# Optimization experiments

Measured on AMD Instinct MI355X. Metric: run time of the kernel, lower is better.

The kernel has to match this reference:

```python
import jax, jax.numpy as jnp
import numpy as np

C = 128
EPS = 1e-5


def _ln(x, g, b):
    m = jnp.mean(x, axis=-1, keepdims=True)
    v = jnp.mean((x - m) ** 2, axis=-1, keepdims=True)
    return (x - m) * jax.lax.rsqrt(v + EPS) * g + b


def setup_inputs() -> dict:
    key = jax.random.key(0)
    ks = jax.random.split(key, 10)
    B, N = 1, 384
    s = 1.0 / np.sqrt(C)
    inp = {
        "z": jax.random.normal(ks[0], (B, N, N, C), dtype=jnp.float32),
        "ln1_g": jnp.ones((C,), jnp.float32),
        "ln1_b": jnp.zeros((C,), jnp.float32),
        "ln2_g": jnp.ones((C,), jnp.float32),
        "ln2_b": jnp.zeros((C,), jnp.float32),
        "Wa": jax.random.uniform(ks[1], (C, C), jnp.float32, -s, s),
        "ba": jnp.zeros((C,), jnp.float32),
        "Wga": jax.random.uniform(ks[2], (C, C), jnp.float32, -s, s),
        "bga": jnp.zeros((C,), jnp.float32),
        "Wb": jax.random.uniform(ks[3], (C, C), jnp.float32, -s, s),
        "bb": jnp.zeros((C,), jnp.float32),
        "Wgb": jax.random.uniform(ks[4], (C, C), jnp.float32, -s, s),
        "bgb": jnp.zeros((C,), jnp.float32),
        "Wg": jax.random.uniform(ks[5], (C, C), jnp.float32, -s, s),
        "bg": jnp.zeros((C,), jnp.float32),
        "Wo": jax.random.uniform(ks[6], (C, C), jnp.float32, -s, s),
        "bo": jnp.zeros((C,), jnp.float32),
    }
    return inp


def reference(z, ln1_g, ln1_b, ln2_g, ln2_b, Wa, ba, Wga, bga, Wb, bb, Wgb, bgb, Wg, bg, Wo, bo):
    # z: (B, i, j, c)
    zn = _ln(z, ln1_g, ln1_b)
    a = (zn @ Wa + ba) * jax.nn.sigmoid(zn @ Wga + bga)      # (B,i,k,c)
    b = (zn @ Wb + bb) * jax.nn.sigmoid(zn @ Wgb + bgb)      # (B,j,k,c)
    gate = jax.nn.sigmoid(zn @ Wg + bg)                      # (B,i,j,c)
    o = jnp.einsum('bikc,bjkc->bijc', a, b)                  # outgoing triangle update
    return gate * (_ln(o, ln2_g, ln2_b) @ Wo + bo)
```

## Files before the change

kernel.cpp:

```cpp
#include <hip/hip_runtime.h>
#include <stdint.h>

typedef _Float16 f16x8 __attribute__((ext_vector_type(8)));
typedef float floatx4 __attribute__((ext_vector_type(4)));

#define RR 147456
#define NC 128
#define NN 384

__device__ inline floatx4 zero4() { floatx4 v; v[0]=0.f; v[1]=0.f; v[2]=0.f; v[3]=0.f; return v; }
__device__ inline float sigmoidf_(float x) { return 1.f / (1.f + __expf(-x)); }

__global__ __launch_bounds__(256) void k0_wt(
    const float* __restrict__ w0, const float* __restrict__ w1,
    const float* __restrict__ w2, const float* __restrict__ w3,
    const float* __restrict__ w4, const float* __restrict__ w5,
    _Float16* __restrict__ wf)
{
  const float* w;
  switch (blockIdx.x) {
    case 0: w = w0; break; case 1: w = w1; break; case 2: w = w2; break;
    case 3: w = w3; break; case 4: w = w4; break; default: w = w5; break;
  }
  _Float16* out = wf + blockIdx.x * 16384;
  const int t = threadIdx.x;
  for (int it = 0; it < 64; ++it) {
    int f = it * 256 + t;
    int j  = f & 7;
    int ln = (f >> 3) & 63;
    int nt = (f >> 9) & 7;
    int k0 = f >> 12;
    int k = k0 * 32 + (ln >> 4) * 8 + j;
    int n = nt * 16 + (ln & 15);
    out[f] = (_Float16)w[k * 128 + n];
  }
}

__global__ __launch_bounds__(256, 4) void k2_ln_gemm(
    const float* __restrict__ z, const float* __restrict__ ln1g, const float* __restrict__ ln1b,
    const _Float16* __restrict__ wf,
    const float* __restrict__ ba, const float* __restrict__ bga,
    const float* __restrict__ bb, const float* __restrict__ bgb,
    const float* __restrict__ bg,
    _Float16* __restrict__ at, _Float16* __restrict__ bt, _Float16* __restrict__ gate)
{
  __shared__ __align__(16) _Float16 zns[64][136];
  const int t = threadIdx.x;
  const int w = t >> 6, lane = t & 63;
  const int l15 = lane & 15, quad = lane >> 4;
  const int r0 = blockIdx.x * 64;
  const int nt0 = w * 2;

  {
    const int g = lane >> 4, h = lane & 15;
    float4 ga = *(const float4*)(ln1g + h*8);
    float4 gb = *(const float4*)(ln1g + h*8 + 4);
    float4 bba = *(const float4*)(ln1b + h*8);
    float4 bbb = *(const float4*)(ln1b + h*8 + 4);
    #pragma unroll
    for (int rr = 0; rr < 4; ++rr) {
      int row = w * 16 + rr * 4 + g;
      const float* zp = z + (size_t)(r0 + row) * NC + h * 8;
      float4 xa = *(const float4*)zp;
      float4 xb = *(const float4*)(zp + 4);
      float s = xa.x + xa.y + xa.z + xa.w + xb.x + xb.y + xb.z + xb.w;
      float q = xa.x*xa.x + xa.y*xa.y + xa.z*xa.z + xa.w*xa.w
              + xb.x*xb.x + xb.y*xb.y + xb.z*xb.z + xb.w*xb.w;
      #pragma unroll
      for (int m = 1; m < 16; m <<= 1) { s += __shfl_xor(s, m); q += __shfl_xor(q, m); }
      float mean = s * (1.f/128.f);
      float var  = q * (1.f/128.f) - mean*mean;
      float rs = rsqrtf(var + 1e-5f);
      union { uint4 u; _Float16 hh[8]; } pk;
      pk.hh[0] = (_Float16)((xa.x - mean) * rs * ga.x + bba.x);
      pk.hh[1] = (_Float16)((xa.y - mean) * rs * ga.y + bba.y);
      pk.hh[2] = (_Float16)((xa.z - mean) * rs * ga.z + bba.z);
      pk.hh[3] = (_Float16)((xa.w - mean) * rs * ga.w + bba.w);
      pk.hh[4] = (_Float16)((xb.x - mean) * rs * gb.x + bbb.x);
      pk.hh[5] = (_Float16)((xb.y - mean) * rs * gb.y + bbb.y);
      pk.hh[6] = (_Float16)((xb.z - mean) * rs * gb.z + bbb.z);
      pk.hh[7] = (_Float16)((xb.w - mean) * rs * gb.w + bbb.w);
      *(uint4*)&zns[row][h * 8] = pk.u;
    }
  }
  __syncthreads();

  const _Float16* pw = wf + lane * 8;
  f16x8 bw[4][2];
  floatx4 acc[4][2];
  union PkU { unsigned int u; _Float16 h[2]; };
  PkU sig[4][2][2];

  auto loadw = [&](int slot) {
    const _Float16* p = pw + slot * 16384;
    #pragma unroll
    for (int k0 = 0; k0 < 4; ++k0)
      #pragma unroll
      for (int j = 0; j < 2; ++j)
        bw[k0][j] = *(const f16x8*)(p + (k0*8 + nt0 + j) * 512);
  };
  auto dogemm = [&]() {
    #pragma unroll
    for (int mt = 0; mt < 4; ++mt) {
      acc[mt][0] = zero4(); acc[mt][1] = zero4();
      #pragma unroll
      for (int k0 = 0; k0 < 4; ++k0) {
        f16x8 af = *(const f16x8*)&zns[mt*16 + l15][k0*32 + quad*8];
        acc[mt][0] = __builtin_amdgcn_mfma_f32_16x16x32_f16(af, bw[k0][0], acc[mt][0], 0, 0, 0);
        acc[mt][1] = __builtin_amdgcn_mfma_f32_16x16x32_f16(af, bw[k0][1], acc[mt][1], 0, 0, 0);
      }
    }
  };
  auto sigpack = [&](const float* big) {
    #pragma unroll
    for (int j = 0; j < 2; ++j) {
      float bgv = big[(nt0 + j)*16 + l15];
      #pragma unroll
      for (int mt = 0; mt < 4; ++mt) {
        sig[mt][j][0].h[0] = (_Float16)sigmoidf_(acc[mt][j][0] + bgv);
        sig[mt][j][0].h[1] = (_Float16)sigmoidf_(acc[mt][j][1] + bgv);
        sig[mt][j][1].h[0] = (_Float16)sigmoidf_(acc[mt][j][2] + bgv);
        sig[mt][j][1].h[1] = (_Float16)sigmoidf_(acc[mt][j][3] + bgv);
      }
    }
  };
  auto combine_store = [&](const float* bia, _Float16* dst) {
    #pragma unroll
    for (int j = 0; j < 2; ++j) {
      int c = (nt0 + j)*16 + l15;
      float bav = bia[c];
      #pragma unroll
      for (int mt = 0; mt < 4; ++mt) {
        union { uint2 u2; _Float16 h[4]; } pk;
        pk.h[0] = (_Float16)((acc[mt][j][0] + bav) * (float)sig[mt][j][0].h[0]);
        pk.h[1] = (_Float16)((acc[mt][j][1] + bav) * (float)sig[mt][j][0].h[1]);
        pk.h[2] = (_Float16)((acc[mt][j][2] + bav) * (float)sig[mt][j][1].h[0]);
        pk.h[3] = (_Float16)((acc[mt][j][3] + bav) * (float)sig[mt][j][1].h[1]);
        *(uint2*)(dst + (size_t)c * RR + r0 + mt*16 + quad*4) = pk.u2;
      }
    }
  };

  loadw(1); dogemm(); sigpack(bga);
  loadw(0); dogemm();
  loadw(3);
  combine_store(ba, at);
  dogemm(); sigpack(bgb);
  loadw(2); dogemm();
  loadw(4);
  combine_store(bb, bt);
  dogemm();
  #pragma unroll
  for (int j = 0; j < 2; ++j) {
    int c = (nt0 + j)*16 + l15;
    float bgv = bg[c];
    #pragma unroll
    for (int mt = 0; mt < 4; ++mt) {
      union { uint2 u2; _Float16 h[4]; } pk;
      #pragma unroll
      for (int r = 0; r < 4; ++r)
        pk.h[r] = (_Float16)sigmoidf_(acc[mt][j][r] + bgv);
      *(uint2*)(gate + (size_t)c * RR + r0 + mt*16 + quad*4) = pk.u2;
    }
  }
}

__global__ __launch_bounds__(256) void k3_tri(
    const _Float16* __restrict__ at, const _Float16* __restrict__ bt, _Float16* __restrict__ o)
{
  __shared__ __align__(16) _Float16 As[128][72];
  __shared__ __align__(16) _Float16 Bs[128][72];
  const int t = threadIdx.x;
  const int w = t >> 6, lane = t & 63, l15 = lane & 15, quad = lane >> 4;
  const int c = blockIdx.y;
  const int i0 = (blockIdx.x / 3) * 128, j0 = (blockIdx.x % 3) * 128;
  const int wi = w >> 1, wj = w & 1;
  const size_t base = (size_t)c * RR;
  const _Float16* A  = at + base;
  const _Float16* Bp = bt + base;

  floatx4 acc[4][4];
  #pragma unroll
  for (int mt = 0; mt < 4; ++mt)
    #pragma unroll
    for (int nt = 0; nt < 4; ++nt) acc[mt][nt] = zero4();

  for (int kk = 0; kk < NN; kk += 64) {
    #pragma unroll
    for (int s2 = 0; s2 < 4; ++s2) {
      int f = s2 * 2048 + t * 8;
      int row = f >> 6, k = f & 63;
      *(uint4*)&As[row][k] = *(const uint4*)(A  + (size_t)(i0 + row) * NN + kk + k);
      *(uint4*)&Bs[row][k] = *(const uint4*)(Bp + (size_t)(j0 + row) * NN + kk + k);
    }
    __syncthreads();
    #pragma unroll
    for (int k0 = 0; k0 < 64; k0 += 32) {
      f16x8 af[4], bfr[4];
      #pragma unroll
      for (int mt = 0; mt < 4; ++mt) af[mt]  = *(const f16x8*)&As[wi*64 + mt*16 + l15][k0 + quad*8];
      #pragma unroll
      for (int nt = 0; nt < 4; ++nt) bfr[nt] = *(const f16x8*)&Bs[wj*64 + nt*16 + l15][k0 + quad*8];
      #pragma unroll
      for (int mt = 0; mt < 4; ++mt)
        #pragma unroll
        for (int nt = 0; nt < 4; ++nt)
          acc[mt][nt] = __builtin_amdgcn_mfma_f32_16x16x32_f16(af[mt], bfr[nt], acc[mt][nt], 0, 0, 0);
    }
    __syncthreads();
  }
  #pragma unroll
  for (int mt = 0; mt < 4; ++mt) {
    #pragma unroll
    for (int r = 0; r < 4; ++r) {
      int i = i0 + wi*64 + mt*16 + quad*4 + r;
      _Float16* orow = o + base + (size_t)i * NN + j0 + wj*64;
      #pragma unroll
      for (int nt = 0; nt < 4; ++nt) orow[nt*16 + l15] = (_Float16)acc[mt][nt][r];
    }
  }
}

__global__ __launch_bounds__(256, 4) void k4_out(
    const _Float16* __restrict__ o, const _Float16* __restrict__ gate,
    const float* __restrict__ ln2g, const float* __restrict__ ln2b,
    const _Float16* __restrict__ wo5, const float* __restrict__ bo,
    float* __restrict__ out)
{
  __shared__ __align__(16) _Float16 osb[64][136];
  const int t = threadIdx.x;
  const int w = t >> 6, lane = t & 63, l15 = lane & 15, quad = lane >> 4;
  const int r0 = blockIdx.x * 64;
  const int nt0 = w * 2;

  #pragma unroll
  for (int it = 0; it < 4; ++it) {
    int f = (it * 256 + t) * 8;
    int cx = f >> 6, p = f & 63;
    f16x8 v = *(const f16x8*)(o + (size_t)cx * RR + r0 + p);
    #pragma unroll
    for (int i = 0; i < 8; ++i) osb[p + i][cx] = v[i];
  }
  __syncthreads();

  {
    const int g = lane >> 4, h = lane & 15;
    float4 ga = *(const float4*)(ln2g + h*8);
    float4 gb = *(const float4*)(ln2g + h*8 + 4);
    float4 bba = *(const float4*)(ln2b + h*8);
    float4 bbb = *(const float4*)(ln2b + h*8 + 4);
    #pragma unroll
    for (int rr = 0; rr < 4; ++rr) {
      int row = w * 16 + rr * 4 + g;
      f16x8 xv = *(const f16x8*)&osb[row][h*8];
      float x0 = (float)xv[0], x1 = (float)xv[1], x2 = (float)xv[2], x3 = (float)xv[3];
      float x4 = (float)xv[4], x5 = (float)xv[5], x6 = (float)xv[6], x7 = (float)xv[7];
      float s = x0+x1+x2+x3+x4+x5+x6+x7;
      float q = x0*x0+x1*x1+x2*x2+x3*x3+x4*x4+x5*x5+x6*x6+x7*x7;
      #pragma unroll
      for (int m = 1; m < 16; m <<= 1) { s += __shfl_xor(s, m); q += __shfl_xor(q, m); }
      float mean = s * (1.f/128.f);
      float var  = q * (1.f/128.f) - mean*mean;
      float rs = rsqrtf(var + 1e-5f);
      union { uint4 u; _Float16 hh[8]; } pk;
      pk.hh[0] = (_Float16)((x0 - mean) * rs * ga.x + bba.x);
      pk.hh[1] = (_Float16)((x1 - mean) * rs * ga.y + bba.y);
      pk.hh[2] = (_Float16)((x2 - mean) * rs * ga.z + bba.z);
      pk.hh[3] = (_Float16)((x3 - mean) * rs * ga.w + bba.w);
      pk.hh[4] = (_Float16)((x4 - mean) * rs * gb.x + bbb.x);
      pk.hh[5] = (_Float16)((x5 - mean) * rs * gb.y + bbb.y);
      pk.hh[6] = (_Float16)((x6 - mean) * rs * gb.z + bbb.z);
      pk.hh[7] = (_Float16)((x7 - mean) * rs * gb.w + bbb.w);
      *(uint4*)&osb[row][h * 8] = pk.u;
    }
  }
  __syncthreads();

  f16x8 bw[4][2];
  {
    const _Float16* p = wo5 + lane * 8;
    #pragma unroll
    for (int k0 = 0; k0 < 4; ++k0)
      #pragma unroll
      for (int j = 0; j < 2; ++j)
        bw[k0][j] = *(const f16x8*)(p + (k0*8 + nt0 + j) * 512);
  }
  floatx4 acc[4][2];
  #pragma unroll
  for (int mt = 0; mt < 4; ++mt) {
    acc[mt][0] = zero4(); acc[mt][1] = zero4();
    #pragma unroll
    for (int k0 = 0; k0 < 4; ++k0) {
      f16x8 af = *(const f16x8*)&osb[mt*16 + l15][k0*32 + quad*8];
      acc[mt][0] = __builtin_amdgcn_mfma_f32_16x16x32_f16(af, bw[k0][0], acc[mt][0], 0, 0, 0);
      acc[mt][1] = __builtin_amdgcn_mfma_f32_16x16x32_f16(af, bw[k0][1], acc[mt][1], 0, 0, 0);
    }
  }

  #pragma unroll
  for (int j = 0; j < 2; ++j) {
    int c = (nt0 + j)*16 + l15;
    float bov = bo[c];
    #pragma unroll
    for (int mt = 0; mt < 4; ++mt) {
      union { uint2 u2; _Float16 h[4]; } gk;
      gk.u2 = *(const uint2*)(gate + (size_t)c * RR + r0 + mt*16 + quad*4);
      #pragma unroll
      for (int r = 0; r < 4; ++r) {
        int rl = mt*16 + quad*4 + r;
        out[(size_t)(r0 + rl) * NC + c] = (float)gk.h[r] * (acc[mt][j][r] + bov);
      }
    }
  }
}

extern "C" void kernel_launch(void* const* d_in, const int* in_sizes, int n_in,
                              void* d_out, int out_size, void* d_ws, size_t ws_size,
                              hipStream_t stream) {
  const float* z    = (const float*)d_in[0];
  const float* l1g  = (const float*)d_in[1];
  const float* l1b  = (const float*)d_in[2];
  const float* l2g  = (const float*)d_in[3];
  const float* l2b  = (const float*)d_in[4];
  const float* Wa   = (const float*)d_in[5];
  const float* ba   = (const float*)d_in[6];
  const float* Wga  = (const float*)d_in[7];
  const float* bga  = (const float*)d_in[8];
  const float* Wb   = (const float*)d_in[9];
  const float* bb   = (const float*)d_in[10];
  const float* Wgb  = (const float*)d_in[11];
  const float* bgb  = (const float*)d_in[12];
  const float* Wg   = (const float*)d_in[13];
  const float* bg   = (const float*)d_in[14];
  const float* Wo   = (const float*)d_in[15];
  const float* bo   = (const float*)d_in[16];

  char* ws = (char*)d_ws;
  _Float16* at_  = (_Float16*)(ws + 0);
  _Float16* bt_  = (_Float16*)(ws + 37748736);
  _Float16* gate = (_Float16*)(ws + 75497472);
  _Float16* o16  = (_Float16*)(ws + 113246208);
  _Float16* wf   = (_Float16*)(ws + 188743680);

  hipLaunchKernelGGL(k0_wt, dim3(6), dim3(256), 0, stream, Wa, Wga, Wb, Wgb, Wg, Wo, wf);
  hipLaunchKernelGGL(k2_ln_gemm, dim3(2304), dim3(256), 0, stream,
                     z, l1g, l1b, wf, ba, bga, bb, bgb, bg, at_, bt_, gate);
  hipLaunchKernelGGL(k3_tri, dim3(9, 128), dim3(256), 0, stream, at_, bt_, o16);
  hipLaunchKernelGGL(k4_out, dim3(2304), dim3(256), 0, stream,
                     o16, gate, l2g, l2b, wf + 5*16384, bo, (float*)d_out);
}
```

Measured before the change: 335.6 us.

## Stage projection stores through LDS and double-buffer the triangle GEMM

The LN+projection kernel now writes its fp16 outputs into a per-wave LDS bounce buffer, then emits 16-byte coalesced stores per channel row instead of scattered 8-byte stores. The triangle-multiply kernel switches to double-buffered 32-wide K tiles with register prefetch of the next global tile while MFMAs run on the current one, and sets launch bounds to 3 blocks per CU. The bounce adds LDS traffic, raises LDS use in k2 and may lower its occupancy. The prefetch registers add register pressure in k3.

```diff
diff --git a/kernel.cpp b/kernel.cpp
--- a/kernel.cpp
+++ b/kernel.cpp
@@ -45,6 +45,7 @@
     _Float16* __restrict__ at, _Float16* __restrict__ bt, _Float16* __restrict__ gate)
 {
   __shared__ __align__(16) _Float16 zns[64][136];
+  __shared__ __align__(16) _Float16 bnc[4][32 * 72];
   const int t = threadIdx.x;
   const int w = t >> 6, lane = t & 63;
   const int l15 = lane & 15, quad = lane >> 4;
@@ -124,6 +125,17 @@
       }
     }
   };
+  auto bounce_out = [&](_Float16* dst) {
+    asm volatile("s_waitcnt lgkmcnt(0)" ::: "memory");
+    const int q2 = lane & 3, cl = lane >> 2;
+    #pragma unroll
+    for (int i = 0; i < 4; ++i) {
+      int cp  = cl + (i >> 1) * 16;
+      int ofs = (i & 1) * 32 + q2 * 8;
+      uint4 v = *(const uint4*)&bnc[w][cp * 72 + ofs];
+      *(uint4*)(dst + (size_t)(w*32 + cp) * RR + r0 + ofs) = v;
+    }
+  };
   auto combine_store = [&](const float* bia, _Float16* dst) {
     #pragma unroll
     for (int j = 0; j < 2; ++j) {
@@ -136,9 +148,10 @@
         pk.h[1] = (_Float16)((acc[mt][j][1] + bav) * (float)sig[mt][j][0].h[1]);
         pk.h[2] = (_Float16)((acc[mt][j][2] + bav) * (float)sig[mt][j][1].h[0]);
         pk.h[3] = (_Float16)((acc[mt][j][3] + bav) * (float)sig[mt][j][1].h[1]);
-        *(uint2*)(dst + (size_t)c * RR + r0 + mt*16 + quad*4) = pk.u2;
+        *(uint2*)&bnc[w][(j*16 + l15) * 72 + mt*16 + quad*4] = pk.u2;
       }
     }
+    bounce_out(dst);
   };
 
   loadw(1); dogemm(); sigpack(bga);
@@ -152,24 +165,24 @@
   dogemm();
   #pragma unroll
   for (int j = 0; j < 2; ++j) {
-    int c = (nt0 + j)*16 + l15;
-    float bgv = bg[c];
+    float bgv = bg[(nt0 + j)*16 + l15];
     #pragma unroll
     for (int mt = 0; mt < 4; ++mt) {
       union { uint2 u2; _Float16 h[4]; } pk;
       #pragma unroll
       for (int r = 0; r < 4; ++r)
         pk.h[r] = (_Float16)sigmoidf_(acc[mt][j][r] + bgv);
-      *(uint2*)(gate + (size_t)c * RR + r0 + mt*16 + quad*4) = pk.u2;
-    }
-  }
-}
-
-__global__ __launch_bounds__(256) void k3_tri(
+      *(uint2*)&bnc[w][(j*16 + l15) * 72 + mt*16 + quad*4] = pk.u2;
+    }
+  }
+  bounce_out(gate);
+}
+
+__global__ __launch_bounds__(256, 3) void k3_tri(
     const _Float16* __restrict__ at, const _Float16* __restrict__ bt, _Float16* __restrict__ o)
 {
-  __shared__ __align__(16) _Float16 As[128][72];
-  __shared__ __align__(16) _Float16 Bs[128][72];
+  __shared__ __align__(16) _Float16 As[2][128 * 40];
+  __shared__ __align__(16) _Float16 Bs[2][128 * 40];
   const int t = threadIdx.x;
   const int w = t >> 6, lane = t & 63, l15 = lane & 15, quad = lane >> 4;
   const int c = blockIdx.y;
@@ -179,36 +192,68 @@
   const _Float16* A  = at + base;
   const _Float16* Bp = bt + base;
 
+  const int srow = t >> 1, sch = (t & 1) * 16;
+  const _Float16* ga = A  + (size_t)(i0 + srow) * NN + sch;
+  const _Float16* gb = Bp + (size_t)(j0 + srow) * NN + sch;
+  _Float16* const pa0 = &As[0][srow * 40 + sch];
+  _Float16* const pb0 = &Bs[0][srow * 40 + sch];
+  _Float16* const pa1 = &As[1][srow * 40 + sch];
+  _Float16* const pb1 = &Bs[1][srow * 40 + sch];
+
   floatx4 acc[4][4];
   #pragma unroll
   for (int mt = 0; mt < 4; ++mt)
     #pragma unroll
     for (int nt = 0; nt < 4; ++nt) acc[mt][nt] = zero4();
 
-  for (int kk = 0; kk < NN; kk += 64) {
-    #pragma unroll
-    for (int s2 = 0; s2 < 4; ++s2) {
-      int f = s2 * 2048 + t * 8;
-      int row = f >> 6, k = f & 63;
-      *(uint4*)&As[row][k] = *(const uint4*)(A  + (size_t)(i0 + row) * NN + kk + k);
-      *(uint4*)&Bs[row][k] = *(const uint4*)(Bp + (size_t)(j0 + row) * NN + kk + k);
-    }
+  f16x8 aP0,aP1,bP0,bP1, aQ0,aQ1,bQ0,bQ1;
+
+  auto gloadP = [&](int kk) {
+    aP0 = *(const f16x8*)(ga + kk); aP1 = *(const f16x8*)(ga + kk + 8);
+    bP0 = *(const f16x8*)(gb + kk); bP1 = *(const f16x8*)(gb + kk + 8);
+  };
+  auto gloadQ = [&](int kk) {
+    aQ0 = *(const f16x8*)(ga + kk); aQ1 = *(const f16x8*)(ga + kk + 8);
+    bQ0 = *(const f16x8*)(gb + kk); bQ1 = *(const f16x8*)(gb + kk + 8);
+  };
+  auto swriteP = [&](int buf) {
+    _Float16* pa = buf ? pa1 : pa0; _Float16* pb = buf ? pb1 : pb0;
+    *(f16x8*)pa = aP0; *(f16x8*)(pa + 8) = aP1;
+    *(f16x8*)pb = bP0; *(f16x8*)(pb + 8) = bP1;
+  };
+  auto swriteQ = [&](int buf) {
+    _Float16* pa = buf ? pa1 : pa0; _Float16* pb = buf ? pb1 : pb0;
+    *(f16x8*)pa = aQ0; *(f16x8*)(pa + 8) = aQ1;
+    *(f16x8*)pb = bQ0; *(f16x8*)(pb + 8) = bQ1;
+  };
+  auto compute = [&](int buf) {
+    f16x8 af[4], bfr[4];
+    #pragma unroll
+    for (int mt = 0; mt < 4; ++mt)
+      af[mt] = *(const f16x8*)&As[buf][(wi*64 + mt*16 + l15) * 40 + quad*8];
+    #pragma unroll
+    for (int nt = 0; nt < 4; ++nt)
+      bfr[nt] = *(const f16x8*)&Bs[buf][(wj*64 + nt*16 + l15) * 40 + quad*8];
+    #pragma unroll
+    for (int mt = 0; mt < 4; ++mt)
+      #pragma unroll
+      for (int nt = 0; nt < 4; ++nt)
+        acc[mt][nt] = __builtin_amdgcn_mfma_f32_16x16x32_f16(af[mt], bfr[nt], acc[mt][nt], 0, 0, 0);
+  };
+
+  gloadP(0); swriteP(0); gloadP(32);
+  __syncthreads();
+  #pragma unroll
+  for (int s = 0; s < 12; s += 2) {
+    if (s + 2 < 12) gloadQ((s + 2) * 32);
+    compute(0);
+    swriteP(1);
     __syncthreads();
-    #pragma unroll
-    for (int k0 = 0; k0 < 64; k0 += 32) {
-      f16x8 af[4], bfr[4];
-      #pragma unroll
-      for (int mt = 0; mt < 4; ++mt) af[mt]  = *(const f16x8*)&As[wi*64 + mt*16 + l15][k0 + quad*8];
-      #pragma unroll
-      for (int nt = 0; nt < 4; ++nt) bfr[nt] = *(const f16x8*)&Bs[wj*64 + nt*16 + l15][k0 + quad*8];
-      #pragma unroll
-      for (int mt = 0; mt < 4; ++mt)
-        #pragma unroll
-        for (int nt = 0; nt < 4; ++nt)
-          acc[mt][nt] = __builtin_amdgcn_mfma_f32_16x16x32_f16(af[mt], bfr[nt], acc[mt][nt], 0, 0, 0);
-    }
-    __syncthreads();
-  }
+    if (s + 3 < 12) gloadP((s + 3) * 32);
+    compute(1);
+    if (s + 2 < 12) { swriteQ(0); __syncthreads(); }
+  }
+
   #pragma unroll
   for (int mt = 0; mt < 4; ++mt) {
     #pragma unroll
@@ -299,16 +344,16 @@
 
   #pragma unroll
   for (int j = 0; j < 2; ++j) {
-    int c = (nt0 + j)*16 + l15;
-    float bov = bo[c];
+    int cch = (nt0 + j)*16 + l15;
+    float bov = bo[cch];
     #pragma unroll
     for (int mt = 0; mt < 4; ++mt) {
       union { uint2 u2; _Float16 h[4]; } gk;
-      gk.u2 = *(const uint2*)(gate + (size_t)c * RR + r0 + mt*16 + quad*4);
+      gk.u2 = *(const uint2*)(gate + (size_t)cch * RR + r0 + mt*16 + quad*4);
       #pragma unroll
       for (int r = 0; r < 4; ++r) {
         int rl = mt*16 + quad*4 + r;
-        out[(size_t)(r0 + rl) * NC + c] = (float)gk.h[r] * (acc[mt][j][r] + bov);
+        out[(size_t)(r0 + rl) * NC + cch] = (float)gk.h[r] * (acc[mt][j][r] + bov);
       }
     }
   }
```

Result: no change. 329.1 us (-1.9%).
